# Optimization experiments

Hardware: AMD Instinct MI355X
Metric: run time of the kernel (lower is better)

## Reference

```python
import jax, jax.numpy as jnp
import numpy as np

N = 1024    # num_points
HID = 1024  # Hamiltonian MLP hidden width


def setup_inputs() -> dict:
    key = jax.random.key(0)
    ks = jax.random.split(key, 6)
    def w(k, shape, fan_in):
        return jax.random.normal(k, shape, dtype=jnp.float32) / np.float32(np.sqrt(fan_in))
    return {
        "x": jax.random.normal(ks[0], (N,), dtype=jnp.float32),
        "q": jax.random.normal(ks[1], (N,), dtype=jnp.float32),
        "p": jax.random.normal(ks[2], (N,), dtype=jnp.float32),
        "W1": w(ks[3], (3 * N, HID), 3 * N),
        "b1": jnp.zeros((HID,), dtype=jnp.float32),
        "W2": w(ks[4], (HID, HID), HID),
        "b2": jnp.zeros((HID,), dtype=jnp.float32),
        "W3": w(ks[5], (HID, 1), HID),
        "b3": jnp.zeros((1,), dtype=jnp.float32),
    }


def _hamiltonian(z, W1, b1, W2, b2, W3, b3):
    # H: R^{3N} -> scalar (matches self.H(cat([x,q,p])).sum())
    h = jnp.tanh(z @ W1 + b1)
    h = jnp.tanh(h @ W2 + b2)
    return jnp.sum(h @ W3 + b3)


def reference(x, q, p, W1, b1, W2, b2, W3, b3):
    n = x.shape[0]

    def grads_qp(x_):
        # (dH/dq, dH/dp) as a function of x, with q,p closed over
        f = lambda q_, p_: _hamiltonian(jnp.concatenate([x_, q_, p_]), W1, b1, W2, b2, W3, b3)
        return jax.grad(f, argnums=(0, 1))(q, p)  # each [n]

    # Diagonal of cross-Hessian blocks via forward-over-reverse, batched over
    # all n basis directions at once (replaces the per-index autograd loop).
    eye = jnp.eye(n, dtype=x.dtype)

    def diag_entry(e_i, i):
        _, (dgq, dgp) = jax.jvp(grads_qp, (x,), (e_i,))
        return dgq[i], dgp[i]  # d2H/(dx_i dq_i), d2H/(dx_i dp_i)

    dH_dq_dx, dH_dp_dx = jax.vmap(diag_entry)(eye, jnp.arange(n))  # each [n]
    return dH_dp_dx, -dH_dq_dx
```

## Files before the change

### kernel.cpp

```cpp
#include <hip/hip_runtime.h>
#include <math.h>

typedef unsigned short u16;
typedef __bf16 bf16x8 __attribute__((ext_vector_type(8)));
typedef float f32x4 __attribute__((ext_vector_type(4)));

__device__ inline u16 bf16_rn(float x) {
    unsigned u = __float_as_uint(x);
    return (u16)((u + 0x7FFFu + ((u >> 16) & 1u)) >> 16);
}
__device__ inline uint2 pack4(u16 a, u16 b, u16 c, u16 d) {
    uint2 r;
    r.x = (unsigned)a | ((unsigned)b << 16);
    r.y = (unsigned)c | ((unsigned)d << 16);
    return r;
}
__device__ inline uint2 pack4f(float a, float b, float c, float d) {
    return pack4(bf16_rn(a), bf16_rn(b), bf16_rn(c), bf16_rn(d));
}
__device__ inline f32x4 mfma16(bf16x8 a, bf16x8 b, f32x4 c) {
    return __builtin_amdgcn_mfma_f32_16x16x32_bf16(a, b, c, 0, 0, 0);
}

__global__ __launch_bounds__(256) void k_pre(const float* __restrict__ x,
                                             const float* __restrict__ q,
                                             const float* __restrict__ p,
                                             const float* __restrict__ W1,
                                             u16* __restrict__ Ah,
                                             float* __restrict__ Upart,
                                             float* __restrict__ out,
                                             float* __restrict__ Vacc) {
    int b = blockIdx.x, t = threadIdx.x;
    if (b < 384) {
        int jc = b;
        int k = (jc & 3) * 256 + t;
        int j0 = (jc >> 2) * 32;
        __shared__ float zs[32];
        if (t < 32) {
            int j = j0 + t;
            zs[t] = (j < 1024) ? x[j] : (j < 2048 ? q[j - 1024] : p[j - 2048]);
        }
        __syncthreads();
        float acc = 0.f;
        if (j0 < 1024) {
#pragma unroll 8
            for (int j = 0; j < 32; ++j) {
                float v = W1[(j0 + j) * 1024 + k];
                Ah[(j0 + j) * 1024 + k] = bf16_rn(v);
                acc += zs[j] * v;
            }
        } else {
#pragma unroll 8
            for (int j = 0; j < 32; ++j) acc += zs[j] * W1[(j0 + j) * 1024 + k];
        }
        Upart[(jc >> 2) * 1024 + k] = acc;
    } else {
        int idx = ((b - 384) * 256 + t) * 4;
        if (idx < 2048) *(float4*)(out + idx) = make_float4(0.f, 0.f, 0.f, 0.f);
        else *(float4*)(Vacc + idx - 2048) = make_float4(0.f, 0.f, 0.f, 0.f);
    }
}

__global__ __launch_bounds__(256) void k_w2v(const float* __restrict__ W2,
                                             const float* __restrict__ b1,
                                             const float* __restrict__ Upart,
                                             float* __restrict__ H1g, float* __restrict__ D1g,
                                             u16* __restrict__ W2h,
                                             u16* __restrict__ WTh,
                                             float* __restrict__ Vacc) {
    __shared__ float T[64][65];
    __shared__ float hs[64], ds[64];
    __shared__ float red[4][64];
    int k0 = blockIdx.y * 64, m0 = blockIdx.x * 64;
    int t = threadIdx.x;
    {
        int lk = t & 63, g = t >> 6;
        float u = 0.f;
#pragma unroll
        for (int c = 0; c < 24; ++c) u += Upart[(g * 24 + c) * 1024 + k0 + lk];
        red[g][lk] = u;
    }
    __syncthreads();
    if (t < 64) {
        float u = red[0][t] + red[1][t] + red[2][t] + red[3][t];
        float h = tanhf(u + b1[k0 + t]);
        hs[t] = h;
        ds[t] = 1.f - h * h;
        if (m0 == 0) { H1g[k0 + t] = h; D1g[k0 + t] = 1.f - h * h; }
    }
    __syncthreads();
    int rr = t >> 4, cc = (t & 15) * 4;
    float4 vp = make_float4(0.f, 0.f, 0.f, 0.f);
#pragma unroll
    for (int j = 0; j < 4; ++j) {
        int r = rr + j * 16;
        float4 v = *(const float4*)(W2 + (k0 + r) * 1024 + m0 + cc);
        T[r][cc + 0] = v.x; T[r][cc + 1] = v.y; T[r][cc + 2] = v.z; T[r][cc + 3] = v.w;
        *(uint2*)&W2h[(k0 + r) * 1024 + m0 + cc] = pack4f(v.x, v.y, v.z, v.w);
        float hk = hs[r];
        vp.x += hk * v.x; vp.y += hk * v.y; vp.z += hk * v.z; vp.w += hk * v.w;
    }
    vp.x += __shfl_xor(vp.x, 16); vp.y += __shfl_xor(vp.y, 16);
    vp.z += __shfl_xor(vp.z, 16); vp.w += __shfl_xor(vp.w, 16);
    vp.x += __shfl_xor(vp.x, 32); vp.y += __shfl_xor(vp.y, 32);
    vp.z += __shfl_xor(vp.z, 32); vp.w += __shfl_xor(vp.w, 32);
    if (((t & 63) >> 4) == 0) {
        atomicAdd(&Vacc[m0 + cc + 0], vp.x);
        atomicAdd(&Vacc[m0 + cc + 1], vp.y);
        atomicAdd(&Vacc[m0 + cc + 2], vp.z);
        atomicAdd(&Vacc[m0 + cc + 3], vp.w);
    }
    __syncthreads();
#pragma unroll
    for (int j = 0; j < 4; ++j) {
        int mrow = rr + j * 16;
        float f0 = T[cc + 0][mrow] * ds[cc + 0];
        float f1 = T[cc + 1][mrow] * ds[cc + 1];
        float f2 = T[cc + 2][mrow] * ds[cc + 2];
        float f3 = T[cc + 3][mrow] * ds[cc + 3];
        *(uint2*)&WTh[(m0 + mrow) * 1024 + k0 + cc] = pack4f(f0, f1, f2, f3);
    }
}

#define LDK 68
__global__ __launch_bounds__(512) void k_gemm1(const u16* __restrict__ Ah,
                                               const u16* __restrict__ Bh,
                                               const float* __restrict__ Vacc,
                                               const float* __restrict__ b2,
                                               const float* __restrict__ W3,
                                               const float* __restrict__ W2,
                                               const float* __restrict__ H1,
                                               const float* __restrict__ D1,
                                               float* __restrict__ Avec,
                                               u16* __restrict__ Sh) {
    __shared__ u16 As[2][64 * LDK];
    __shared__ u16 Bs[2][64 * LDK];
    __shared__ float sv[1024];
    int tid = threadIdx.x;
    if (blockIdx.x == 16) {
        int kbase = blockIdx.y * 64;
#pragma unroll
        for (int j = 0; j < 2; ++j) {
            int m = tid + j * 512;
            float h = tanhf(Vacc[m] + b2[m]);
            sv[m] = (1.f - h * h) * W3[m];
        }
        __syncthreads();
        int g = tid >> 3, sub = tid & 7;
        int k = kbase + g;
        const float* wrow = W2 + k * 1024 + sub * 128;
        const float* svp = sv + sub * 128;
        float acc = 0.f;
#pragma unroll 8
        for (int j = 0; j < 128; ++j) acc += wrow[j] * svp[j];
        acc += __shfl_xor(acc, 1);
        acc += __shfl_xor(acc, 2);
        acc += __shfl_xor(acc, 4);
        if (sub == 0) Avec[k] = -2.f * H1[k] * D1[k] * acc;
        return;
    }
    int lane = tid & 63, wv = tid >> 6;
    int kh = wv >> 2, wy = (wv >> 1) & 1, wx = wv & 1;
    int i0 = blockIdx.y * 64, m0 = blockIdx.x * 64;
    int srow = tid >> 3, sseg = (tid & 7) * 8;
    int ldso = srow * LDK + sseg;
    const u16* ap = Ah + (i0 + srow) * 1024 + sseg;
    const u16* bp = Bh + (m0 + srow) * 1024 + sseg;
    int tx = lane & 15, qy = lane >> 4;
    int koff = kh * 32 + qy * 8;
    int raA[2], rbB[2];
    raA[0] = (wy * 32 + tx) * LDK + koff;
    raA[1] = raA[0] + 16 * LDK;
    rbB[0] = (wx * 32 + tx) * LDK + koff;
    rbB[1] = rbB[0] + 16 * LDK;
    f32x4 acc[2][2];
#pragma unroll
    for (int a = 0; a < 2; ++a)
#pragma unroll
        for (int b = 0; b < 2; ++b) acc[a][b] = (f32x4){0.f, 0.f, 0.f, 0.f};

    uint4 pa1 = *(const uint4*)(ap + 64);
    uint4 pc1 = *(const uint4*)(bp + 64);
    *(uint4*)&As[0][ldso] = *(const uint4*)(ap);
    *(uint4*)&Bs[0][ldso] = *(const uint4*)(bp);

    for (int k0 = 0; k0 < 1024; k0 += 64) {
        int buf = (k0 >> 6) & 1;
        int kn2 = (k0 + 128) & 1023;
        uint4 pa2 = *(const uint4*)(ap + kn2);
        uint4 pc2 = *(const uint4*)(bp + kn2);
        __syncthreads();
        bf16x8 aH0 = *(const bf16x8*)&As[buf][raA[0]];
        bf16x8 aH1 = *(const bf16x8*)&As[buf][raA[1]];
        bf16x8 bH0 = *(const bf16x8*)&Bs[buf][rbB[0]];
        bf16x8 bH1 = *(const bf16x8*)&Bs[buf][rbB[1]];
        acc[0][0] = mfma16(aH0, bH0, acc[0][0]);
        acc[0][1] = mfma16(aH0, bH1, acc[0][1]);
        acc[1][0] = mfma16(aH1, bH0, acc[1][0]);
        acc[1][1] = mfma16(aH1, bH1, acc[1][1]);
        int nb = buf ^ 1;
        *(uint4*)&As[nb][ldso] = pa1;
        *(uint4*)&Bs[nb][ldso] = pc1;
        pa1 = pa2; pc1 = pc2;
    }
    __syncthreads();
    f32x4* mrg = (f32x4*)&As[0][0];
    if (kh == 1) {
#pragma unroll
        for (int si = 0; si < 2; ++si)
#pragma unroll
            for (int sj = 0; sj < 2; ++sj)
                mrg[(((wy * 2 + wx) * 4 + si * 2 + sj) * 4 + qy) * 16 + tx] = acc[si][sj];
    }
    __syncthreads();
    if (kh == 0) {
#pragma unroll
        for (int si = 0; si < 2; ++si)
#pragma unroll
            for (int sj = 0; sj < 2; ++sj) {
                f32x4 o = mrg[(((wy * 2 + wx) * 4 + si * 2 + sj) * 4 + qy) * 16 + tx];
                acc[si][sj][0] += o[0]; acc[si][sj][1] += o[1];
                acc[si][sj][2] += o[2]; acc[si][sj][3] += o[3];
            }
#pragma unroll
        for (int sj = 0; sj < 2; ++sj) {
            int m = m0 + wx * 32 + sj * 16 + tx;
            float hv = tanhf(Vacc[m] + b2[m]);
            float d2 = 1.f - hv * hv;
            float cm = -2.f * hv * d2 * W3[m];
#pragma unroll
            for (int si = 0; si < 2; ++si) {
                int ib = i0 + wy * 32 + si * 16 + qy * 4;
#pragma unroll
                for (int r = 0; r < 4; ++r)
                    Sh[(ib + r) * 1024 + m] = bf16_rn(acc[si][sj][r] * cm);
            }
        }
    }
}

__global__ __launch_bounds__(512) void k_gemm2(const u16* __restrict__ Sh,
                                               const u16* __restrict__ W2h,
                                               const float* __restrict__ W1,
                                               const float* __restrict__ D1,
                                               const float* __restrict__ Avec,
                                               float* __restrict__ out) {
    __shared__ u16 As[2][64 * LDK];
    __shared__ u16 Bs[2][64 * LDK];
    int tid = threadIdx.x, lane = tid & 63, wv = tid >> 6;
    int kh = wv >> 2, wy = (wv >> 1) & 1, wx = wv & 1;
    int i0 = blockIdx.y * 64, k0g = blockIdx.x * 64;
    int srow = tid >> 3, sseg = (tid & 7) * 8;
    int ldso = srow * LDK + sseg;
    const u16* ap = Sh + (i0 + srow) * 1024 + sseg;
    const u16* bp = W2h + (k0g + srow) * 1024 + sseg;
    int tx = lane & 15, qy = lane >> 4;
    int koff = kh * 32 + qy * 8;
    int raA[2], rbB[2];
    raA[0] = (wy * 32 + tx) * LDK + koff;
    raA[1] = raA[0] + 16 * LDK;
    rbB[0] = (wx * 32 + tx) * LDK + koff;
    rbB[1] = rbB[0] + 16 * LDK;
    f32x4 acc[2][2];
#pragma unroll
    for (int a = 0; a < 2; ++a)
#pragma unroll
        for (int b = 0; b < 2; ++b) acc[a][b] = (f32x4){0.f, 0.f, 0.f, 0.f};

    uint4 pa1 = *(const uint4*)(ap + 64);
    uint4 pc1 = *(const uint4*)(bp + 64);
    *(uint4*)&As[0][ldso] = *(const uint4*)(ap);
    *(uint4*)&Bs[0][ldso] = *(const uint4*)(bp);

    for (int m0 = 0; m0 < 1024; m0 += 64) {
        int buf = (m0 >> 6) & 1;
        int mn2 = (m0 + 128) & 1023;
        uint4 pa2 = *(const uint4*)(ap + mn2);
        uint4 pc2 = *(const uint4*)(bp + mn2);
        __syncthreads();
        bf16x8 aH0 = *(const bf16x8*)&As[buf][raA[0]];
        bf16x8 aH1 = *(const bf16x8*)&As[buf][raA[1]];
        bf16x8 bH0 = *(const bf16x8*)&Bs[buf][rbB[0]];
        bf16x8 bH1 = *(const bf16x8*)&Bs[buf][rbB[1]];
        acc[0][0] = mfma16(aH0, bH0, acc[0][0]);
        acc[0][1] = mfma16(aH0, bH1, acc[0][1]);
        acc[1][0] = mfma16(aH1, bH0, acc[1][0]);
        acc[1][1] = mfma16(aH1, bH1, acc[1][1]);
        int nb = buf ^ 1;
        *(uint4*)&As[nb][ldso] = pa1;
        *(uint4*)&Bs[nb][ldso] = pc1;
        pa1 = pa2; pc1 = pc2;
    }
    __syncthreads();
    f32x4* mrg = (f32x4*)&As[0][0];
    if (kh == 1) {
#pragma unroll
        for (int si = 0; si < 2; ++si)
#pragma unroll
            for (int sj = 0; sj < 2; ++sj)
                mrg[(((wy * 2 + wx) * 4 + si * 2 + sj) * 4 + qy) * 16 + tx] = acc[si][sj];
    }
    __syncthreads();
    if (kh == 0) {
#pragma unroll
        for (int si = 0; si < 2; ++si)
#pragma unroll
            for (int sj = 0; sj < 2; ++sj) {
                f32x4 o = mrg[(((wy * 2 + wx) * 4 + si * 2 + sj) * 4 + qy) * 16 + tx];
                acc[si][sj][0] += o[0]; acc[si][sj][1] += o[1];
                acc[si][sj][2] += o[2]; acc[si][sj][3] += o[3];
            }
        int kk[2];
        float d1v[2], avv[2];
#pragma unroll
        for (int sj = 0; sj < 2; ++sj) {
            kk[sj] = k0g + wx * 32 + sj * 16 + tx;
            d1v[sj] = D1[kk[sj]];
            avv[sj] = Avec[kk[sj]];
        }
#pragma unroll
        for (int si = 0; si < 2; ++si) {
            int ib = i0 + wy * 32 + si * 16 + qy * 4;
#pragma unroll
            for (int r = 0; r < 4; ++r) {
                int i = ib + r;
                float pq = 0.f, pp = 0.f;
#pragma unroll
                for (int sj = 0; sj < 2; ++sj) {
                    int k = kk[sj];
                    float dr = avv[sj] * W1[i * 1024 + k] + d1v[sj] * acc[si][sj][r];
                    pq += W1[(1024 + i) * 1024 + k] * dr;
                    pp += W1[(2048 + i) * 1024 + k] * dr;
                }
                for (int o = 1; o < 16; o <<= 1) {
                    pq += __shfl_xor(pq, o);
                    pp += __shfl_xor(pp, o);
                }
                if (tx == 0) {
                    atomicAdd(&out[i], pp);
                    atomicAdd(&out[1024 + i], -pq);
                }
            }
        }
    }
}

extern "C" void kernel_launch(void* const* d_in, const int* in_sizes, int n_in,
                              void* d_out, int out_size, void* d_ws, size_t ws_size,
                              hipStream_t stream) {
    const float* x = (const float*)d_in[0];
    const float* q = (const float*)d_in[1];
    const float* p = (const float*)d_in[2];
    const float* W1 = (const float*)d_in[3];
    const float* b1 = (const float*)d_in[4];
    const float* W2 = (const float*)d_in[5];
    const float* b2 = (const float*)d_in[6];
    const float* W3 = (const float*)d_in[7];
    float* out = (float*)d_out;
    float* ws = (float*)d_ws;
    float* H1 = ws, *D1 = ws + 1024, *Avec = ws + 2048, *Vacc = ws + 3072;
    float* Upart = ws + 4096;
    u16* u0 = (u16*)(ws + 131072);
    u16* Ah = u0;
    u16* WTh = u0 + 1048576;
    u16* W2h = u0 + 2097152;
    u16* Sh = u0 + 3145728;

    k_pre<<<387, 256, 0, stream>>>(x, q, p, W1, Ah, Upart, out, Vacc);
    k_w2v<<<dim3(16, 16), 256, 0, stream>>>(W2, b1, Upart, H1, D1, W2h, WTh, Vacc);
    k_gemm1<<<dim3(17, 16), 512, 0, stream>>>(Ah, WTh, Vacc, b2, W3, W2, H1, D1, Avec, Sh);
    k_gemm2<<<dim3(16, 16), 512, 0, stream>>>(Sh, W2h, W1, D1, Avec, out);
}
```

Before: 115.3 us.

## Fuse pre and W2 prep kernels using inter-block completion flags

Merges the W1 partial-product kernel and the W2 conversion/transpose kernel into one launch. The W2 blocks first load W2 and write its bf16 copy, then spin on per-block release flags until every pre block has finished before reading Upart. This removes one launch boundary and overlaps W2 loading with the W1 reduction. The flags are set to a fixed magic value and never reset, so on repeated calls the wait can pass on stale flags and race with the zeroing of Vacc. The spin also assumes all pre blocks get scheduled ahead of or alongside the waiting blocks.

```diff
diff --git a/kernel.cpp b/kernel.cpp
--- a/kernel.cpp
+++ b/kernel.cpp
@@ -2,8 +2,11 @@
 #include <math.h>
 
 typedef unsigned short u16;
+typedef unsigned long long u64;
 typedef __bf16 bf16x8 __attribute__((ext_vector_type(8)));
 typedef float f32x4 __attribute__((ext_vector_type(4)));
+
+#define MAGIC 0xA5C3F00D9E1B7D42ULL
 
 __device__ inline u16 bf16_rn(float x) {
     unsigned u = __float_as_uint(x);
@@ -22,62 +25,85 @@
     return __builtin_amdgcn_mfma_f32_16x16x32_bf16(a, b, c, 0, 0, 0);
 }
 
-__global__ __launch_bounds__(256) void k_pre(const float* __restrict__ x,
-                                             const float* __restrict__ q,
-                                             const float* __restrict__ p,
-                                             const float* __restrict__ W1,
-                                             u16* __restrict__ Ah,
-                                             float* __restrict__ Upart,
-                                             float* __restrict__ out,
-                                             float* __restrict__ Vacc) {
-    int b = blockIdx.x, t = threadIdx.x;
-    if (b < 384) {
-        int jc = b;
-        int k = (jc & 3) * 256 + t;
-        int j0 = (jc >> 2) * 32;
-        __shared__ float zs[32];
-        if (t < 32) {
-            int j = j0 + t;
-            zs[t] = (j < 1024) ? x[j] : (j < 2048 ? q[j - 1024] : p[j - 2048]);
-        }
-        __syncthreads();
-        float acc = 0.f;
-        if (j0 < 1024) {
-#pragma unroll 8
-            for (int j = 0; j < 32; ++j) {
-                float v = W1[(j0 + j) * 1024 + k];
-                Ah[(j0 + j) * 1024 + k] = bf16_rn(v);
-                acc += zs[j] * v;
-            }
-        } else {
-#pragma unroll 8
-            for (int j = 0; j < 32; ++j) acc += zs[j] * W1[(j0 + j) * 1024 + k];
-        }
-        Upart[(jc >> 2) * 1024 + k] = acc;
-    } else {
-        int idx = ((b - 384) * 256 + t) * 4;
-        if (idx < 2048) *(float4*)(out + idx) = make_float4(0.f, 0.f, 0.f, 0.f);
-        else *(float4*)(Vacc + idx - 2048) = make_float4(0.f, 0.f, 0.f, 0.f);
-    }
-}
-
-__global__ __launch_bounds__(256) void k_w2v(const float* __restrict__ W2,
-                                             const float* __restrict__ b1,
-                                             const float* __restrict__ Upart,
-                                             float* __restrict__ H1g, float* __restrict__ D1g,
-                                             u16* __restrict__ W2h,
-                                             u16* __restrict__ WTh,
-                                             float* __restrict__ Vacc) {
+__global__ __launch_bounds__(256) void k_prew2v(
+    const float* __restrict__ x, const float* __restrict__ q, const float* __restrict__ p,
+    const float* __restrict__ W1, const float* __restrict__ b1, const float* __restrict__ W2,
+    u16* __restrict__ Ah, u16* __restrict__ W2h, u16* __restrict__ WTh,
+    float* __restrict__ Upart, float* __restrict__ out, float* __restrict__ Vacc,
+    float* __restrict__ H1g, float* __restrict__ D1g, u64* __restrict__ done) {
     __shared__ float T[64][65];
     __shared__ float hs[64], ds[64];
     __shared__ float red[4][64];
-    int k0 = blockIdx.y * 64, m0 = blockIdx.x * 64;
-    int t = threadIdx.x;
+    __shared__ float zs[32];
+    int b = blockIdx.x, t = threadIdx.x;
+
+    if (b < 387) {
+        if (b < 384) {
+            int jc = b;
+            int k = (jc & 3) * 256 + t;
+            int j0 = (jc >> 2) * 32;
+            if (t < 32) {
+                int j = j0 + t;
+                zs[t] = (j < 1024) ? x[j] : (j < 2048 ? q[j - 1024] : p[j - 2048]);
+            }
+            __syncthreads();
+            float acc = 0.f;
+            if (j0 < 1024) {
+#pragma unroll 8
+                for (int j = 0; j < 32; ++j) {
+                    float v = W1[(j0 + j) * 1024 + k];
+                    Ah[(j0 + j) * 1024 + k] = bf16_rn(v);
+                    acc += zs[j] * v;
+                }
+            } else {
+#pragma unroll 8
+                for (int j = 0; j < 32; ++j) acc += zs[j] * W1[(j0 + j) * 1024 + k];
+            }
+            Upart[(jc >> 2) * 1024 + k] = acc;
+        } else {
+            int idx = ((b - 384) * 256 + t) * 4;
+            if (idx < 2048) *(float4*)(out + idx) = make_float4(0.f, 0.f, 0.f, 0.f);
+            else *(float4*)(Vacc + idx - 2048) = make_float4(0.f, 0.f, 0.f, 0.f);
+        }
+        __syncthreads();
+        if (t == 0) {
+            __threadfence();
+            __hip_atomic_store(&done[b], MAGIC, __ATOMIC_RELEASE, __HIP_MEMORY_SCOPE_AGENT);
+        }
+        return;
+    }
+
+    int c = b - 387;
+    int k0 = (c >> 4) * 64, m0 = (c & 15) * 64;
+    int rr = t >> 4, cc = (t & 15) * 4;
+    float4 va[4];
+#pragma unroll
+    for (int j = 0; j < 4; ++j) {
+        int r = rr + j * 16;
+        float4 v = *(const float4*)(W2 + (k0 + r) * 1024 + m0 + cc);
+        va[j] = v;
+        T[r][cc + 0] = v.x; T[r][cc + 1] = v.y; T[r][cc + 2] = v.z; T[r][cc + 3] = v.w;
+        *(uint2*)&W2h[(k0 + r) * 1024 + m0 + cc] = pack4f(v.x, v.y, v.z, v.w);
+    }
+    for (;;) {
+        int mine = 1;
+        {
+            u64 v0 = __hip_atomic_load(&done[t], __ATOMIC_RELAXED, __HIP_MEMORY_SCOPE_AGENT);
+            mine = (v0 == MAGIC);
+        }
+        if (t + 256 < 387) {
+            u64 v1 = __hip_atomic_load(&done[t + 256], __ATOMIC_RELAXED, __HIP_MEMORY_SCOPE_AGENT);
+            mine = mine && (v1 == MAGIC);
+        }
+        if (__syncthreads_and(mine)) break;
+        __builtin_amdgcn_s_sleep(8);
+    }
+    __threadfence();
     {
         int lk = t & 63, g = t >> 6;
         float u = 0.f;
 #pragma unroll
-        for (int c = 0; c < 24; ++c) u += Upart[(g * 24 + c) * 1024 + k0 + lk];
+        for (int c2 = 0; c2 < 24; ++c2) u += Upart[(g * 24 + c2) * 1024 + k0 + lk];
         red[g][lk] = u;
     }
     __syncthreads();
@@ -89,16 +115,11 @@
         if (m0 == 0) { H1g[k0 + t] = h; D1g[k0 + t] = 1.f - h * h; }
     }
     __syncthreads();
-    int rr = t >> 4, cc = (t & 15) * 4;
     float4 vp = make_float4(0.f, 0.f, 0.f, 0.f);
 #pragma unroll
     for (int j = 0; j < 4; ++j) {
-        int r = rr + j * 16;
-        float4 v = *(const float4*)(W2 + (k0 + r) * 1024 + m0 + cc);
-        T[r][cc + 0] = v.x; T[r][cc + 1] = v.y; T[r][cc + 2] = v.z; T[r][cc + 3] = v.w;
-        *(uint2*)&W2h[(k0 + r) * 1024 + m0 + cc] = pack4f(v.x, v.y, v.z, v.w);
-        float hk = hs[r];
-        vp.x += hk * v.x; vp.y += hk * v.y; vp.z += hk * v.z; vp.w += hk * v.w;
+        float hk = hs[rr + j * 16];
+        vp.x += hk * va[j].x; vp.y += hk * va[j].y; vp.z += hk * va[j].z; vp.w += hk * va[j].w;
     }
     vp.x += __shfl_xor(vp.x, 16); vp.y += __shfl_xor(vp.y, 16);
     vp.z += __shfl_xor(vp.z, 16); vp.w += __shfl_xor(vp.w, 16);
@@ -110,7 +131,6 @@
         atomicAdd(&Vacc[m0 + cc + 2], vp.z);
         atomicAdd(&Vacc[m0 + cc + 3], vp.w);
     }
-    __syncthreads();
 #pragma unroll
     for (int j = 0; j < 4; ++j) {
         int mrow = rr + j * 16;
@@ -360,14 +380,15 @@
     float* ws = (float*)d_ws;
     float* H1 = ws, *D1 = ws + 1024, *Avec = ws + 2048, *Vacc = ws + 3072;
     float* Upart = ws + 4096;
+    u64* done = (u64*)(ws + 102400);
     u16* u0 = (u16*)(ws + 131072);
     u16* Ah = u0;
     u16* WTh = u0 + 1048576;
     u16* W2h = u0 + 2097152;
     u16* Sh = u0 + 3145728;
 
-    k_pre<<<387, 256, 0, stream>>>(x, q, p, W1, Ah, Upart, out, Vacc);
-    k_w2v<<<dim3(16, 16), 256, 0, stream>>>(W2, b1, Upart, H1, D1, W2h, WTh, Vacc);
+    k_prew2v<<<643, 256, 0, stream>>>(x, q, p, W1, b1, W2, Ah, W2h, WTh,
+                                      Upart, out, Vacc, H1, D1, done);
     k_gemm1<<<dim3(17, 16), 512, 0, stream>>>(Ah, WTh, Vacc, b2, W3, W2, H1, D1, Avec, Sh);
     k_gemm2<<<dim3(16, 16), 512, 0, stream>>>(Sh, W2h, W1, D1, Avec, out);
 }
```

Result: slower. 147.4 us (+27.8%).
